# Performance work log

Measured on AMD Instinct MI355X. Metric: run time of the kernel, lower is better.

## Reference

```python
import jax, jax.numpy as jnp
import numpy as np

ACT_GUARD = 2.0   # 2 ** act_guard_bit (act_guard_bit = 1)
WGT_GUARD = 2.0   # 2 ** weight_guard_bit (weight_guard_bit = 1)


def _ste_round(v):
    # straight-through estimator round (QNMethod.STE)
    return v + jax.lax.stop_gradient(jnp.round(v) - v)


def setup_inputs() -> dict:
    key = jax.random.key(0)
    k_x, k_w, k_b = jax.random.split(key, 3)
    B, S, DIN, DOUT = 4, 2048, 2048, 8192
    ACT_INIT_S, ACT_INIT_Q, LOG_S_INIT = -10.0, 10.0, -8.0
    x = jax.random.normal(k_x, (B, S, DIN), dtype=jnp.float32)
    weight = jax.random.normal(k_w, (DOUT, DIN), dtype=jnp.float32) * 0.02
    bias = jax.random.normal(k_b, (DOUT,), dtype=jnp.float32) * 0.01
    log_act_s = jnp.full((1,), ACT_INIT_S, dtype=jnp.float32)
    log_act_q = jnp.full((1,), ACT_INIT_Q, dtype=jnp.float32)
    act_b = jnp.full((1,), -jnp.exp2(ACT_INIT_Q - 1.0), dtype=jnp.float32)  # -512
    log_wght_s = jnp.full((DOUT, 1), LOG_S_INIT, dtype=jnp.float32)
    return {"x": x, "weight": weight, "bias": bias, "log_act_s": log_act_s,
            "log_act_q": log_act_q, "act_b": act_b, "log_wght_s": log_wght_s}


def reference(x, weight, bias, log_act_s, log_act_q, act_b, log_wght_s):
    # --- activation fake-quant (per-tensor) ---
    s = jnp.exp2(log_act_s)                       # [1]
    q = jnp.exp2(log_act_q)                       # [1]
    zp = jnp.round(act_b / s * ACT_GUARD) / ACT_GUARD * s  # guard-bit rounded zero point
    lo, hi = zp, zp + q - s
    qx = _ste_round((jnp.clip(x, lo, hi) - zp) / s)
    x_dq = qx * s + zp                            # dequantized activations

    # --- weight fake-quant (per-channel over out dim, amin/amax over dim 1) ---
    w_scale = jnp.exp2(log_wght_s)                # [DOUT, 1]
    wmin = jnp.min(weight, axis=1, keepdims=True)
    wmax = jnp.max(weight, axis=1, keepdims=True)
    qwmin = jnp.round(wmin / w_scale * WGT_GUARD) / WGT_GUARD * w_scale
    qwmax = jnp.round(wmax / w_scale * WGT_GUARD) / WGT_GUARD * w_scale
    qw = _ste_round((jnp.clip(weight, qwmin, qwmax) - qwmin) / w_scale)
    w_dq = qw * w_scale + qwmin                   # dequantized weights

    # --- affine: y = x @ W.T + b ---
    return jnp.einsum('bsi,oi->bso', x_dq, w_dq) + bias
```

## Files before the change

kernel.cpp:

```cpp
#include <hip/hip_runtime.h>
#include <hip/hip_bf16.h>


using f16x8 = __attribute__((ext_vector_type(8))) _Float16;
using f32x4 = __attribute__((ext_vector_type(4))) float;

#define AS1 __attribute__((address_space(1)))
#define AS3 __attribute__((address_space(3)))

static __device__ __forceinline__ void gload_lds16(const void* g, void* l) {
    __builtin_amdgcn_global_load_lds((const AS1 void*)g, (AS3 void*)l, 16, 0, 0);
}

__global__ __launch_bounds__(256) void quant_kernel(
    const float* __restrict__ X,
    const float* __restrict__ las, const float* __restrict__ laq,
    const float* __restrict__ ab,
    const float* __restrict__ W, const float* __restrict__ lws,
    _Float16* __restrict__ Xq, _Float16* __restrict__ Wq) {
    constexpr int K = 2048;
    __shared__ float smn[4], smx[4];
    const int t = threadIdx.x;

    if (blockIdx.x < 8192) {
        const float ls = las[0], lq = laq[0];
        const float s = exp2f(ls);
        const float rs = exp2f(-ls);
        const float q = exp2f(lq);
        const float zp = rintf(ab[0] * rs * 2.0f) * 0.5f * s;
        const float lo = zp;
        const float hi = (zp + q) - s;

        const size_t base = ((size_t)blockIdx.x * 256 + t) * 8;
        float4 v0 = *(const float4*)&X[base];
        float4 v1 = *(const float4*)&X[base + 4];
        float vals[8] = {v0.x, v0.y, v0.z, v0.w, v1.x, v1.y, v1.z, v1.w};

        f16x8 out;
#pragma unroll
        for (int i = 0; i < 8; ++i) {
            float c = fminf(fmaxf(vals[i], lo), hi);
            float qx = rintf((c - zp) * rs);
            out[i] = (_Float16)(qx * s + zp);
        }
        *(f16x8*)&Xq[base] = out;
    } else {
        const int row = blockIdx.x - 8192;
        const float* w = W + (size_t)row * K;

        float4 v0 = ((const float4*)w)[t * 2];
        float4 v1 = ((const float4*)w)[t * 2 + 1];
        float vals[8] = {v0.x, v0.y, v0.z, v0.w, v1.x, v1.y, v1.z, v1.w};

        float mn = vals[0], mx = vals[0];
#pragma unroll
        for (int i = 1; i < 8; ++i) {
            mn = fminf(mn, vals[i]);
            mx = fmaxf(mx, vals[i]);
        }
#pragma unroll
        for (int off = 32; off >= 1; off >>= 1) {
            mn = fminf(mn, __shfl_xor(mn, off));
            mx = fmaxf(mx, __shfl_xor(mx, off));
        }
        if ((t & 63) == 0) { smn[t >> 6] = mn; smx[t >> 6] = mx; }
        __syncthreads();
        mn = fminf(fminf(smn[0], smn[1]), fminf(smn[2], smn[3]));
        mx = fmaxf(fmaxf(smx[0], smx[1]), fmaxf(smx[2], smx[3]));

        const float l = lws[row];
        const float ws = exp2f(l);
        const float rs = exp2f(-l);
        const float qwmin = rintf(mn * rs * 2.0f) * 0.5f * ws;
        const float qwmax = rintf(mx * rs * 2.0f) * 0.5f * ws;

        f16x8 out;
#pragma unroll
        for (int i = 0; i < 8; ++i) {
            float c = fminf(fmaxf(vals[i], qwmin), qwmax);
            float qw = rintf((c - qwmin) * rs);
            out[i] = (_Float16)(qw * ws + qwmin);
        }
        *(f16x8*)&Wq[(size_t)row * K + (size_t)t * 8] = out;
    }
}

__global__ __launch_bounds__(512, 2) void gemm_kernel(
    const _Float16* __restrict__ A, const _Float16* __restrict__ B,
    const float* __restrict__ bias, float* __restrict__ C) {
    constexpr int N = 8192, K = 2048;
    constexpr int KT = K / 64;
    __shared__ char smem[131072];

    const int bid = blockIdx.x;
    const int j = bid >> 3;
    const int bm = (bid & 7) * 4 + (j & 3);
    const int bn = j >> 2;

    const int t = threadIdx.x;
    const int lane = t & 63;
    const int wid = t >> 6;
    const int wr = wid >> 2;
    const int wc = wid & 3;
    const int l15 = lane & 15;
    const int lq = lane >> 4;

    const int d0 = t * 16, d1 = d0 + 8192;
    const int r0 = d0 >> 7, c0 = (((d0 & 127) ^ (((d0 >> 7) & 7) << 4)) >> 1);
    const int r1 = d1 >> 7, c1 = (((d1 & 127) ^ (((d1 >> 7) & 7) << 4)) >> 1);
    const _Float16* Agb = A + (size_t)bm * 256 * K;
    const _Float16* Bgb = B + (size_t)bn * 256 * K;

    const int cp0 = (lq * 16) ^ ((l15 & 7) << 4);
    const int cp1 = cp0 ^ 64;

    f32x4 acc[8][4] = {};
    f16x8 fA[8][2], fB[4][2];

#define STAGEH(GB, RO, DBS, H, KS) do {                                        \
        const _Float16* _g = (GB) + (size_t)((H) * 128) * K + (size_t)(KS) * 64;\
        char* _l = smem + (RO) + ((DBS) * 2 + (H)) * 16384;                    \
        gload_lds16(_g + (size_t)r0 * K + c0, _l + d0);                        \
        gload_lds16(_g + (size_t)r1 * K + c1, _l + d1);                        \
    } while (0)

#define STAGET(DBS, KS) do {                                                   \
        STAGEH(Agb, 0,     DBS, 0, KS);                                        \
        STAGEH(Agb, 0,     DBS, 1, KS);                                        \
        STAGEH(Bgb, 65536, DBS, 0, KS);                                        \
        STAGEH(Bgb, 65536, DBS, 1, KS);                                        \
    } while (0)

    STAGET(0, 0);
    asm volatile("s_waitcnt vmcnt(0)" ::: "memory");
    __builtin_amdgcn_s_barrier();

    for (int kt = 0; kt < KT; ++kt) {
        const int db = kt & 1;
        const int nx = (kt + 1 < KT) ? kt + 1 : KT - 1;

        STAGET(db ^ 1, nx);

        const char* _a = smem + (db * 2 + wr) * 16384 + l15 * 128;
        const char* _b = smem + 65536 + (db * 2 + (wc >> 1)) * 16384 +
                         (wc & 1) * 8192 + l15 * 128;
#pragma unroll
        for (int m = 0; m < 8; ++m)
            fA[m][0] = *(const f16x8*)(_a + m * 2048 + cp0);
#pragma unroll
        for (int n = 0; n < 4; ++n)
            fB[n][0] = *(const f16x8*)(_b + n * 2048 + cp0);
#pragma unroll
        for (int m = 0; m < 8; ++m)
            fA[m][1] = *(const f16x8*)(_a + m * 2048 + cp1);
#pragma unroll
        for (int n = 0; n < 4; ++n)
            fB[n][1] = *(const f16x8*)(_b + n * 2048 + cp1);

#pragma unroll
        for (int m = 0; m < 8; ++m)
#pragma unroll
            for (int n = 0; n < 4; ++n)
                acc[m][n] = __builtin_amdgcn_mfma_f32_16x16x32_f16(
                    fA[m][0], fB[n][0], acc[m][n], 0, 0, 0);
#pragma unroll
        for (int m = 0; m < 8; ++m)
#pragma unroll
            for (int n = 0; n < 4; ++n)
                acc[m][n] = __builtin_amdgcn_mfma_f32_16x16x32_f16(
                    fA[m][1], fB[n][1], acc[m][n], 0, 0, 0);

        asm volatile("s_waitcnt vmcnt(0)" ::: "memory");
        __builtin_amdgcn_s_barrier();
    }
#undef STAGEH
#undef STAGET

#pragma unroll
    for (int m = 0; m < 8; ++m) {
        const int row = bm * 256 + wr * 128 + m * 16 + lq * 4;
#pragma unroll
        for (int n = 0; n < 4; ++n) {
            const int col = bn * 256 + wc * 64 + n * 16 + l15;
            const float bv = bias[col];
#pragma unroll
            for (int r = 0; r < 4; ++r) {
                C[(size_t)(row + r) * N + col] = acc[m][n][r] + bv;
            }
        }
    }
}

extern "C" void kernel_launch(void* const* d_in, const int* in_sizes, int n_in,
                              void* d_out, int out_size, void* d_ws, size_t ws_size,
                              hipStream_t stream) {
    const float* x    = (const float*)d_in[0];
    const float* w    = (const float*)d_in[1];
    const float* bias = (const float*)d_in[2];
    const float* las  = (const float*)d_in[3];
    const float* laq  = (const float*)d_in[4];
    const float* ab   = (const float*)d_in[5];
    const float* lws  = (const float*)d_in[6];
    float* out = (float*)d_out;

    constexpr size_t MK = (size_t)8192 * 2048;
    _Float16* xq = (_Float16*)d_ws;
    _Float16* wq = (_Float16*)((char*)d_ws + MK * sizeof(_Float16));

    quant_kernel<<<16384, 256, 0, stream>>>(x, las, laq, ab, w, lws, xq, wq);
    gemm_kernel<<<1024, 512, 0, stream>>>(xq, wq, bias, out);
}
```

Before: 279.0 us.

## Switch GEMM to 32x32x16 MFMA with fragment-ordered LDS layout

Replaces the 16x16x32 MFMA tiling with 32x32x16 MFMA instructions, so each wave computes its 128x64 tile with 8 accumulators of 16 floats instead of 32 of 4. The global-to-LDS staging is remapped so each 64-lane chunk lands in LDS already in the per-lane fragment order, which makes the LDS reads contiguous lane*16 loads and removes the XOR swizzle. The goal is fewer MFMA issues and lower LDS read overhead per K step. Contiguous per-lane reads should avoid bank conflicts, but the global loads now gather 16-byte pieces spread across rows, which may reduce coalescing.

```diff
diff --git a/kernel.cpp b/kernel.cpp
--- a/kernel.cpp
+++ b/kernel.cpp
@@ -2,8 +2,8 @@
 #include <hip/hip_bf16.h>
 
 
-using f16x8 = __attribute__((ext_vector_type(8))) _Float16;
-using f32x4 = __attribute__((ext_vector_type(4))) float;
+using f16x8  = __attribute__((ext_vector_type(8))) _Float16;
+using f32x16 = __attribute__((ext_vector_type(16))) float;
 
 #define AS1 __attribute__((address_space(1)))
 #define AS3 __attribute__((address_space(3)))
@@ -102,33 +102,37 @@
     const int wid = t >> 6;
     const int wr = wid >> 2;
     const int wc = wid & 3;
-    const int l15 = lane & 15;
-    const int lq = lane >> 4;
-
-    const int d0 = t * 16, d1 = d0 + 8192;
-    const int r0 = d0 >> 7, c0 = (((d0 & 127) ^ (((d0 >> 7) & 7) << 4)) >> 1);
-    const int r1 = d1 >> 7, c1 = (((d1 & 127) ^ (((d1 >> 7) & 7) << 4)) >> 1);
+    const int l31 = lane & 31;
+    const int lh = lane >> 5;
+
     const _Float16* Agb = A + (size_t)bm * 256 * K;
     const _Float16* Bgb = B + (size_t)bn * 256 * K;
 
-    const int cp0 = (lq * 16) ^ ((l15 & 7) << 4);
-    const int cp1 = cp0 ^ 64;
-
-    f32x4 acc[8][4] = {};
-    f16x8 fA[8][2], fB[4][2];
-
-#define STAGEH(GB, RO, DBS, H, KS) do {                                        \
-        const _Float16* _g = (GB) + (size_t)((H) * 128) * K + (size_t)(KS) * 64;\
-        char* _l = smem + (RO) + ((DBS) * 2 + (H)) * 16384;                    \
-        gload_lds16(_g + (size_t)r0 * K + c0, _l + d0);                        \
-        gload_lds16(_g + (size_t)r1 * K + c1, _l + d1);                        \
-    } while (0)
+    int goffA[4], goffB[4];
+#pragma unroll
+    for (int i = 0; i < 4; ++i) {
+        const int c = t + i * 512;
+        const int s = c >> 6;
+        const int ln = c & 63;
+        const int kk = (s & 3) * 16 + (ln >> 5) * 8;
+        const int rowA = (s >> 4) * 128 + ((s >> 2) & 3) * 32 + (ln & 31);
+        goffA[i] = rowA * K + kk;
+        const int rowB = (s >> 3) * 64 + ((s >> 2) & 1) * 32 + (ln & 31);
+        goffB[i] = rowB * K + kk;
+    }
+
+    f32x16 acc[4][2] = {};
+    f16x8 fa[4][4], fb[2][4];
 
 #define STAGET(DBS, KS) do {                                                   \
-        STAGEH(Agb, 0,     DBS, 0, KS);                                        \
-        STAGEH(Agb, 0,     DBS, 1, KS);                                        \
-        STAGEH(Bgb, 65536, DBS, 0, KS);                                        \
-        STAGEH(Bgb, 65536, DBS, 1, KS);                                        \
+        _Pragma("unroll")                                                      \
+        for (int _i = 0; _i < 4; ++_i)                                         \
+            gload_lds16(Agb + goffA[_i] + (KS) * 64,                           \
+                        smem + (DBS) * 32768 + (t + _i * 512) * 16);           \
+        _Pragma("unroll")                                                      \
+        for (int _i = 0; _i < 4; ++_i)                                         \
+            gload_lds16(Bgb + goffB[_i] + (KS) * 64,                           \
+                        smem + 65536 + (DBS) * 32768 + (t + _i * 512) * 16);   \
     } while (0)
 
     STAGET(0, 0);
@@ -141,51 +145,43 @@
 
         STAGET(db ^ 1, nx);
 
-        const char* _a = smem + (db * 2 + wr) * 16384 + l15 * 128;
-        const char* _b = smem + 65536 + (db * 2 + (wc >> 1)) * 16384 +
-                         (wc & 1) * 8192 + l15 * 128;
-#pragma unroll
-        for (int m = 0; m < 8; ++m)
-            fA[m][0] = *(const f16x8*)(_a + m * 2048 + cp0);
-#pragma unroll
-        for (int n = 0; n < 4; ++n)
-            fB[n][0] = *(const f16x8*)(_b + n * 2048 + cp0);
-#pragma unroll
-        for (int m = 0; m < 8; ++m)
-            fA[m][1] = *(const f16x8*)(_a + m * 2048 + cp1);
-#pragma unroll
-        for (int n = 0; n < 4; ++n)
-            fB[n][1] = *(const f16x8*)(_b + n * 2048 + cp1);
-
-#pragma unroll
-        for (int m = 0; m < 8; ++m)
-#pragma unroll
-            for (int n = 0; n < 4; ++n)
-                acc[m][n] = __builtin_amdgcn_mfma_f32_16x16x32_f16(
-                    fA[m][0], fB[n][0], acc[m][n], 0, 0, 0);
-#pragma unroll
-        for (int m = 0; m < 8; ++m)
-#pragma unroll
-            for (int n = 0; n < 4; ++n)
-                acc[m][n] = __builtin_amdgcn_mfma_f32_16x16x32_f16(
-                    fA[m][1], fB[n][1], acc[m][n], 0, 0, 0);
+        const char* baseA = smem + db * 32768 + wr * 16384 + lane * 16;
+        const char* baseB = smem + 65536 + db * 32768 + wc * 8192 + lane * 16;
+#pragma unroll
+        for (int ks = 0; ks < 4; ++ks) {
+#pragma unroll
+            for (int m = 0; m < 4; ++m)
+                fa[m][ks] = *(const f16x8*)(baseA + (m * 4 + ks) * 1024);
+#pragma unroll
+            for (int n = 0; n < 2; ++n)
+                fb[n][ks] = *(const f16x8*)(baseB + (n * 4 + ks) * 1024);
+        }
+
+#pragma unroll
+        for (int ks = 0; ks < 4; ++ks)
+#pragma unroll
+            for (int m = 0; m < 4; ++m)
+#pragma unroll
+                for (int n = 0; n < 2; ++n)
+                    acc[m][n] = __builtin_amdgcn_mfma_f32_32x32x16_f16(
+                        fa[m][ks], fb[n][ks], acc[m][n], 0, 0, 0);
 
         asm volatile("s_waitcnt vmcnt(0)" ::: "memory");
         __builtin_amdgcn_s_barrier();
     }
-#undef STAGEH
 #undef STAGET
 
 #pragma unroll
-    for (int m = 0; m < 8; ++m) {
-        const int row = bm * 256 + wr * 128 + m * 16 + lq * 4;
-#pragma unroll
-        for (int n = 0; n < 4; ++n) {
-            const int col = bn * 256 + wc * 64 + n * 16 + l15;
+    for (int m = 0; m < 4; ++m) {
+        const int row0 = bm * 256 + wr * 128 + m * 32 + 4 * lh;
+#pragma unroll
+        for (int n = 0; n < 2; ++n) {
+            const int col = bn * 256 + wc * 64 + n * 32 + l31;
             const float bv = bias[col];
 #pragma unroll
-            for (int r = 0; r < 4; ++r) {
-                C[(size_t)(row + r) * N + col] = acc[m][n][r] + bv;
+            for (int r = 0; r < 16; ++r) {
+                const int row = row0 + (r & 3) + 8 * (r >> 2);
+                C[(size_t)row * N + col] = acc[m][n][r] + bv;
             }
         }
     }
```

New measurement: 384.4 us. 37.8% more time.

## Use 4-slot K=32 LDS ring with two-tile-ahead prefetch in GEMM

Applied to the files above, without the earlier changes.

Halves the K-step per iteration to 32 and turns the double-buffered LDS into a four-slot ring, so global-to-LDS loads are issued two tiles ahead and only the older batch is waited on with vmcnt(4). The swizzle and fragment addressing are reworked for 64-byte rows. Less data is in flight per stage, which should hide global latency better, but the loop now runs twice as many iterations with twice as many barriers. Slot reuse may race, because the load for kt+2 is issued before the barrier that guards slot reads.

```diff
diff --git a/kernel.cpp b/kernel.cpp
--- a/kernel.cpp
+++ b/kernel.cpp
@@ -89,7 +89,7 @@
     const _Float16* __restrict__ A, const _Float16* __restrict__ B,
     const float* __restrict__ bias, float* __restrict__ C) {
     constexpr int N = 8192, K = 2048;
-    constexpr int KT = K / 64;
+    constexpr int KT = K / 32;
     __shared__ char smem[131072];
 
     const int bid = blockIdx.x;
@@ -106,75 +106,67 @@
     const int lq = lane >> 4;
 
     const int d0 = t * 16, d1 = d0 + 8192;
-    const int r0 = d0 >> 7, c0 = (((d0 & 127) ^ (((d0 >> 7) & 7) << 4)) >> 1);
-    const int r1 = d1 >> 7, c1 = (((d1 & 127) ^ (((d1 >> 7) & 7) << 4)) >> 1);
+    const int r0 = d0 >> 6, c0e = (((d0 & 63) ^ (((d0 >> 9) & 1) << 5)) >> 1);
+    const int r1 = d1 >> 6, c1e = (((d1 & 63) ^ (((d1 >> 9) & 1) << 5)) >> 1);
     const _Float16* Agb = A + (size_t)bm * 256 * K;
     const _Float16* Bgb = B + (size_t)bn * 256 * K;
 
-    const int cp0 = (lq * 16) ^ ((l15 & 7) << 4);
-    const int cp1 = cp0 ^ 64;
+    const int cp = (lq * 16) ^ ((l15 & 8) << 2);
 
     f32x4 acc[8][4] = {};
-    f16x8 fA[8][2], fB[4][2];
-
-#define STAGEH(GB, RO, DBS, H, KS) do {                                        \
-        const _Float16* _g = (GB) + (size_t)((H) * 128) * K + (size_t)(KS) * 64;\
-        char* _l = smem + (RO) + ((DBS) * 2 + (H)) * 16384;                    \
-        gload_lds16(_g + (size_t)r0 * K + c0, _l + d0);                        \
-        gload_lds16(_g + (size_t)r1 * K + c1, _l + d1);                        \
+    f16x8 fA[8], fB[4];
+
+#define STAGET(SLOT, KS) do {                                                  \
+        const _Float16* _ga = Agb + (size_t)(KS) * 32;                         \
+        char* _la = smem + (SLOT) * 16384;                                     \
+        gload_lds16(_ga + (size_t)r0 * K + c0e, _la + d0);                     \
+        gload_lds16(_ga + (size_t)r1 * K + c1e, _la + d1);                     \
+        const _Float16* _gb = Bgb + (size_t)(KS) * 32;                         \
+        char* _lb = smem + 65536 + (SLOT) * 16384;                             \
+        gload_lds16(_gb + (size_t)r0 * K + c0e, _lb + d0);                     \
+        gload_lds16(_gb + (size_t)r1 * K + c1e, _lb + d1);                     \
     } while (0)
 
-#define STAGET(DBS, KS) do {                                                   \
-        STAGEH(Agb, 0,     DBS, 0, KS);                                        \
-        STAGEH(Agb, 0,     DBS, 1, KS);                                        \
-        STAGEH(Bgb, 65536, DBS, 0, KS);                                        \
-        STAGEH(Bgb, 65536, DBS, 1, KS);                                        \
-    } while (0)
+#define SB() __builtin_amdgcn_sched_barrier(0)
 
     STAGET(0, 0);
-    asm volatile("s_waitcnt vmcnt(0)" ::: "memory");
+    STAGET(1, 1);
+    SB();
+    asm volatile("s_waitcnt vmcnt(4)");
+    SB();
     __builtin_amdgcn_s_barrier();
 
     for (int kt = 0; kt < KT; ++kt) {
-        const int db = kt & 1;
-        const int nx = (kt + 1 < KT) ? kt + 1 : KT - 1;
-
-        STAGET(db ^ 1, nx);
-
-        const char* _a = smem + (db * 2 + wr) * 16384 + l15 * 128;
-        const char* _b = smem + 65536 + (db * 2 + (wc >> 1)) * 16384 +
-                         (wc & 1) * 8192 + l15 * 128;
+        const int slot = kt & 3;
+        const int nslot = (kt + 2) & 3;
+        const int nx = (kt + 2 < KT) ? kt + 2 : KT - 1;
+
+        STAGET(nslot, nx);
+
+        const char* _a = smem + slot * 16384 + (wr * 128 + l15) * 64 + cp;
+        const char* _b = smem + 65536 + slot * 16384 +
+                         (wc * 64 + l15) * 64 + cp;
 #pragma unroll
         for (int m = 0; m < 8; ++m)
-            fA[m][0] = *(const f16x8*)(_a + m * 2048 + cp0);
+            fA[m] = *(const f16x8*)(_a + m * 1024);
 #pragma unroll
         for (int n = 0; n < 4; ++n)
-            fB[n][0] = *(const f16x8*)(_b + n * 2048 + cp0);
-#pragma unroll
-        for (int m = 0; m < 8; ++m)
-            fA[m][1] = *(const f16x8*)(_a + m * 2048 + cp1);
-#pragma unroll
-        for (int n = 0; n < 4; ++n)
-            fB[n][1] = *(const f16x8*)(_b + n * 2048 + cp1);
+            fB[n] = *(const f16x8*)(_b + n * 1024);
 
 #pragma unroll
         for (int m = 0; m < 8; ++m)
 #pragma unroll
             for (int n = 0; n < 4; ++n)
                 acc[m][n] = __builtin_amdgcn_mfma_f32_16x16x32_f16(
-                    fA[m][0], fB[n][0], acc[m][n], 0, 0, 0);
-#pragma unroll
-        for (int m = 0; m < 8; ++m)
-#pragma unroll
-            for (int n = 0; n < 4; ++n)
-                acc[m][n] = __builtin_amdgcn_mfma_f32_16x16x32_f16(
-                    fA[m][1], fB[n][1], acc[m][n], 0, 0, 0);
-
-        asm volatile("s_waitcnt vmcnt(0)" ::: "memory");
+                    fA[m], fB[n], acc[m][n], 0, 0, 0);
+
+        SB();
+        asm volatile("s_waitcnt vmcnt(4)");
+        SB();
         __builtin_amdgcn_s_barrier();
     }
-#undef STAGEH
 #undef STAGET
+#undef SB
 
 #pragma unroll
     for (int m = 0; m < 8; ++m) {
```

Result: slower. 302.3 us (+8.4%).
